# Kernel optimization log

Measured on AMD Instinct MI355X. Metric: run time of the kernel, lower is better.

The kernel has to match this reference:

```python
import jax, jax.numpy as jnp
import numpy as np

WINDOW_SIZE = 11
SIGMA = 1.5
C1 = 0.01 ** 2
C2 = 0.03 ** 2


def _create_window(window_size, channel, dtype):
    coords = jnp.arange(window_size, dtype=jnp.float32) - window_size // 2
    g = jnp.exp(-coords ** 2 / (2.0 * SIGMA ** 2))
    g = g / g.sum()
    win2d = jnp.outer(g, g)  # [k, k]
    # depthwise kernel: [C, 1, k, k] in OIHW with feature_group_count=C
    return jnp.broadcast_to(win2d[None, None], (channel, 1, window_size, window_size)).astype(dtype)


def _dw_conv(x, w, channel):
    pad = WINDOW_SIZE // 2
    return jax.lax.conv_general_dilated(
        x, w,
        window_strides=(1, 1),
        padding=[(pad, pad), (pad, pad)],
        dimension_numbers=('NCHW', 'OIHW', 'NCHW'),
        feature_group_count=channel,
    )


def setup_inputs() -> dict:
    key = jax.random.key(0)
    k1, k2 = jax.random.split(key)
    shape = (16, 3, 512, 512)
    img1 = jax.random.uniform(k1, shape, dtype=jnp.float32)
    img2 = jax.random.uniform(k2, shape, dtype=jnp.float32)
    return {"img1": img1, "img2": img2}


def reference(img1, img2):
    channel = img1.shape[1]
    window = _create_window(WINDOW_SIZE, channel, img1.dtype)

    mu1 = _dw_conv(img1, window, channel)
    mu2 = _dw_conv(img2, window, channel)
    mu1_sq = mu1 * mu1
    mu2_sq = mu2 * mu2
    mu1_mu2 = mu1 * mu2

    sigma1_sq = _dw_conv(img1 * img1, window, channel) - mu1_sq
    sigma2_sq = _dw_conv(img2 * img2, window, channel) - mu2_sq
    sigma12 = _dw_conv(img1 * img2, window, channel) - mu1_mu2

    ssim_map = ((2.0 * mu1_mu2 + C1) * (2.0 * sigma12 + C2)) / (
        (mu1_sq + mu2_sq + C1) * (sigma1_sq + sigma2_sq + C2))
    # forward() returns only the mean SSIM (mcs mean is computed but discarded)
    return ssim_map.mean()
```

## Files before the change

kernel.cpp:

```cpp
#include <hip/hip_runtime.h>
#include <math.h>


#define KW 11
#define RAD 5
#define IMG_W 512
#define IMG_H 512
#define TY 34
#define NJB 4
#define LROW 74
#define C1F 0.0001f
#define C2F 0.0009f

typedef float v2f __attribute__((ext_vector_type(2)));

__global__ __launch_bounds__(256) void ssim_fused_kernel(
    const float* __restrict__ img1,
    const float* __restrict__ img2,
    float* __restrict__ out,
    float inv_n)
{
    __shared__ v2f rows[4][2][LROW];
    __shared__ float red[4];

    const int tid  = threadIdx.x;
    const int lane = tid & 63;
    const int wvi  = tid >> 6;

    const int x0 = (blockIdx.x * 4 + wvi) * 64;
    const int y0 = blockIdx.y * TY;

    const size_t pbase = (size_t)blockIdx.z * (size_t)(IMG_W * IMG_H);
    const float* __restrict__ p1 = img1 + pbase;
    const float* __restrict__ p2 = img2 + pbase;

    float g[KW];
    {
        double t[KW];
        double s = 0.0;
        #pragma unroll
        for (int i = 0; i < KW; ++i) {
            const double c = (double)(i - RAD);
            t[i] = exp(-(c * c) / 4.5);
            s += t[i];
        }
        #pragma unroll
        for (int i = 0; i < KW; ++i) {
            const float gi = (float)(t[i] / s);
            g[i] = __int_as_float(__builtin_amdgcn_readfirstlane(__float_as_int(gi)));
        }
    }

    const int c0   = x0 - RAD + lane;
    const int c0c  = min(max(c0, 0), IMG_W - 1);
    const float m0 = (c0 == c0c) ? 1.f : 0.f;
    const int c1   = c0 + 64;
    const int c1c  = min(max(c1, 0), IMG_W - 1);
    const float m1 = (c1 == c1c) ? 1.f : 0.f;

    auto load_row = [&](int j, v2f& v0, v2f& v1) {
        const int ir = y0 - RAD + j;
        v0 = (v2f){0.f, 0.f};
        v1 = (v2f){0.f, 0.f};
        if ((unsigned)ir < (unsigned)IMG_H) {
            const float* r1 = p1 + ir * IMG_W;
            const float* r2 = p2 + ir * IMG_W;
            v0.x = r1[c0c] * m0;
            v0.y = r2[c0c] * m0;
            if (lane < 2 * RAD) {
                v1.x = r1[c1c] * m1;
                v1.y = r2[c1c] * m1;
            }
        }
    };

    v2f  accMu[KW], accSq[KW];
    float accXy[KW];
    #pragma unroll
    for (int s = 0; s < KW; ++s) {
        accMu[s] = (v2f){0.f, 0.f};
        accSq[s] = (v2f){0.f, 0.f};
        accXy[s] = 0.f;
    }

    v2f cur0, cur1;
    load_row(0, cur0, cur1);

    float acc = 0.f;

    #pragma clang loop unroll(disable)
    for (int jb = 0; jb < NJB; ++jb) {
        #pragma unroll
        for (int P = 0; P < KW; ++P) {
            const int j   = jb * KW + P;
            const int buf = j & 1;
            v2f* __restrict__ wrow = rows[wvi][buf];

            wrow[lane] = cur0;
            if (lane < 2 * RAD) wrow[64 + lane] = cur1;
            __threadfence_block();

            load_row(j + 1, cur0, cur1);

            v2f hmu = (v2f){0.f, 0.f};
            v2f hsq = (v2f){0.f, 0.f};
            float hxy = 0.f;
            #pragma unroll
            for (int k = 0; k < KW; ++k) {
                const v2f ab = wrow[lane + k];
                const v2f w  = g[k] * ab;
                hmu += w;
                hsq = __builtin_elementwise_fma(w, ab, hsq);
                hxy = fmaf(w.x, ab.y, hxy);
            }

            #pragma unroll
            for (int s = 0; s < KW; ++s) {
                const float wt = g[(P - s + KW) % KW];
                const v2f wv2 = (v2f){wt, wt};
                if (s == P) {
                    accMu[s] = wv2 * hmu;
                    accSq[s] = wv2 * hsq;
                    accXy[s] = wt * hxy;
                } else {
                    accMu[s] = __builtin_elementwise_fma(wv2, hmu, accMu[s]);
                    accSq[s] = __builtin_elementwise_fma(wv2, hsq, accSq[s]);
                    accXy[s] = fmaf(wt, hxy, accXy[s]);
                }
            }

            const int oy = y0 + j - 2 * RAD;
            if (j >= 2 * RAD && oy < IMG_H) {
                const int e = (P + 1) % KW;
                const v2f mu    = accMu[e];
                const v2f musq  = mu * mu;
                const float mu12 = mu.x * mu.y;
                const v2f sig   = accSq[e] - musq;
                const float s12 = accXy[e] - mu12;
                const float num = fmaf(2.f, mu12, C1F) * fmaf(2.f, s12, C2F);
                const float den = (musq.x + musq.y + C1F) * (sig.x + sig.y + C2F);
                acc = fmaf(num, __builtin_amdgcn_rcpf(den), acc);
            }
        }
    }

    #pragma unroll
    for (int off = 32; off > 0; off >>= 1)
        acc += __shfl_xor(acc, off, 64);
    if (lane == 0) red[wvi] = acc;
    __syncthreads();
    if (tid == 0) {
        const float s = red[0] + red[1] + red[2] + red[3];
        atomicAdd(out, s * inv_n);
    }
}

extern "C" void kernel_launch(void* const* d_in, const int* in_sizes, int n_in,
                              void* d_out, int out_size, void* d_ws, size_t ws_size,
                              hipStream_t stream) {
    (void)in_sizes; (void)n_in; (void)d_ws; (void)ws_size;
    const float* img1 = (const float*)d_in[0];
    const float* img2 = (const float*)d_in[1];
    float* out = (float*)d_out;

    hipMemsetAsync(out, 0, (size_t)out_size * sizeof(float), stream);

    const float inv_n = 1.0f / (16.0f * 3.0f * 512.0f * 512.0f);
    dim3 grid(2, 16, 16 * 3);
    ssim_fused_kernel<<<grid, dim3(256, 1, 1), 0, stream>>>(img1, img2, out, inv_n);
}
```

Before: 175.2 us.

## Compute two output columns per thread with vectorized loads and summed squares

Each lane now handles two adjacent output columns, so a wave covers 128 columns and a block spans the full image width. Rows are loaded as float2 pairs and staged in LDS as float4, which halves the number of LDS reads per output. Only x²+y² and x·y are accumulated, since SSIM needs only the sum of the two variances, so the separate xx and yy sums are merged. The grid shrinks to 16x48 blocks, which halves the block count. It adds register pressure from four accumulator sets of eleven slots each, which may lower occupancy.

```diff
diff --git a/kernel.cpp b/kernel.cpp
--- a/kernel.cpp
+++ b/kernel.cpp
@@ -8,11 +8,12 @@
 #define IMG_H 512
 #define TY 34
 #define NJB 4
-#define LROW 74
+#define NV4 70
 #define C1F 0.0001f
 #define C2F 0.0009f
 
 typedef float v2f __attribute__((ext_vector_type(2)));
+typedef float v4f __attribute__((ext_vector_type(4)));
 
 __global__ __launch_bounds__(256) void ssim_fused_kernel(
     const float* __restrict__ img1,
@@ -20,17 +21,17 @@
     float* __restrict__ out,
     float inv_n)
 {
-    __shared__ v2f rows[4][2][LROW];
+    __shared__ v4f rows[4][2][NV4];
     __shared__ float red[4];
 
     const int tid  = threadIdx.x;
     const int lane = tid & 63;
     const int wvi  = tid >> 6;
 
-    const int x0 = (blockIdx.x * 4 + wvi) * 64;
-    const int y0 = blockIdx.y * TY;
+    const int x0 = wvi * 128;
+    const int y0 = blockIdx.x * TY;
 
-    const size_t pbase = (size_t)blockIdx.z * (size_t)(IMG_W * IMG_H);
+    const size_t pbase = (size_t)blockIdx.y * (size_t)(IMG_W * IMG_H);
     const float* __restrict__ p1 = img1 + pbase;
     const float* __restrict__ p2 = img2 + pbase;
 
@@ -51,40 +52,42 @@
         }
     }
 
-    const int c0   = x0 - RAD + lane;
-    const int c0c  = min(max(c0, 0), IMG_W - 1);
-    const float m0 = (c0 == c0c) ? 1.f : 0.f;
-    const int c1   = c0 + 64;
-    const int c1c  = min(max(c1, 0), IMG_W - 1);
-    const float m1 = (c1 == c1c) ? 1.f : 0.f;
+    const int cm  = x0 - 6 + 2 * lane;
+    const int cmc = min(max(cm, 0), IMG_W - 2);
+    const float mm0 = (cm     >= 0 && cm     < IMG_W) ? 1.f : 0.f;
+    const float mm1 = (cm + 1 >= 0 && cm + 1 < IMG_W) ? 1.f : 0.f;
+    const int ch  = x0 + 122 + 2 * lane;
+    const int chc = min(max(ch, 0), IMG_W - 2);
+    const float mh0 = (ch     < IMG_W) ? 1.f : 0.f;
+    const float mh1 = (ch + 1 < IMG_W) ? 1.f : 0.f;
 
-    auto load_row = [&](int j, v2f& v0, v2f& v1) {
+    auto load_row = [&](int j, v4f& vm, v4f& vh) {
         const int ir = y0 - RAD + j;
-        v0 = (v2f){0.f, 0.f};
-        v1 = (v2f){0.f, 0.f};
+        vm = (v4f){0.f, 0.f, 0.f, 0.f};
+        vh = (v4f){0.f, 0.f, 0.f, 0.f};
         if ((unsigned)ir < (unsigned)IMG_H) {
             const float* r1 = p1 + ir * IMG_W;
             const float* r2 = p2 + ir * IMG_W;
-            v0.x = r1[c0c] * m0;
-            v0.y = r2[c0c] * m0;
-            if (lane < 2 * RAD) {
-                v1.x = r1[c1c] * m1;
-                v1.y = r2[c1c] * m1;
+            const v2f a = *reinterpret_cast<const v2f*>(r1 + cmc);
+            const v2f b = *reinterpret_cast<const v2f*>(r2 + cmc);
+            vm = (v4f){a.x * mm0, b.x * mm0, a.y * mm1, b.y * mm1};
+            if (lane < 6) {
+                const v2f ah = *reinterpret_cast<const v2f*>(r1 + chc);
+                const v2f bh = *reinterpret_cast<const v2f*>(r2 + chc);
+                vh = (v4f){ah.x * mh0, bh.x * mh0, ah.y * mh1, bh.y * mh1};
             }
         }
     };
 
-    v2f  accMu[KW], accSq[KW];
-    float accXy[KW];
+    v2f aMuA[KW], aSPA[KW], aMuB[KW], aSPB[KW];
     #pragma unroll
     for (int s = 0; s < KW; ++s) {
-        accMu[s] = (v2f){0.f, 0.f};
-        accSq[s] = (v2f){0.f, 0.f};
-        accXy[s] = 0.f;
+        aMuA[s] = (v2f){0.f, 0.f}; aSPA[s] = (v2f){0.f, 0.f};
+        aMuB[s] = (v2f){0.f, 0.f}; aSPB[s] = (v2f){0.f, 0.f};
     }
 
-    v2f cur0, cur1;
-    load_row(0, cur0, cur1);
+    v4f curm, curh;
+    load_row(0, curm, curh);
 
     float acc = 0.f;
 
@@ -94,24 +97,40 @@
         for (int P = 0; P < KW; ++P) {
             const int j   = jb * KW + P;
             const int buf = j & 1;
-            v2f* __restrict__ wrow = rows[wvi][buf];
+            v4f* __restrict__ wrow = rows[wvi][buf];
 
-            wrow[lane] = cur0;
-            if (lane < 2 * RAD) wrow[64 + lane] = cur1;
+            wrow[lane] = curm;
+            if (lane < 6) wrow[64 + lane] = curh;
             __threadfence_block();
 
-            load_row(j + 1, cur0, cur1);
+            load_row(j + 1, curm, curh);
 
-            v2f hmu = (v2f){0.f, 0.f};
-            v2f hsq = (v2f){0.f, 0.f};
-            float hxy = 0.f;
+            v4f e[7];
+            #pragma unroll
+            for (int r = 0; r < 7; ++r) e[r] = wrow[lane + r];
+
+            v2f ab[14], sp[14];
+            #pragma unroll
+            for (int i = 0; i < 14; ++i) {
+                const v4f q = e[i >> 1];
+                const v2f t = (i & 1) ? (v2f){q.z, q.w} : (v2f){q.x, q.y};
+                ab[i] = t;
+            }
+            #pragma unroll
+            for (int i = 1; i <= 12; ++i) {
+                const v2f t = ab[i];
+                sp[i] = (v2f){fmaf(t.x, t.x, t.y * t.y), t.x * t.y};
+            }
+
+            v2f hMuA = (v2f){0.f, 0.f}, hSPA = (v2f){0.f, 0.f};
+            v2f hMuB = (v2f){0.f, 0.f}, hSPB = (v2f){0.f, 0.f};
             #pragma unroll
             for (int k = 0; k < KW; ++k) {
-                const v2f ab = wrow[lane + k];
-                const v2f w  = g[k] * ab;
-                hmu += w;
-                hsq = __builtin_elementwise_fma(w, ab, hsq);
-                hxy = fmaf(w.x, ab.y, hxy);
+                const v2f gk = (v2f){g[k], g[k]};
+                hMuA = __builtin_elementwise_fma(gk, ab[1 + k], hMuA);
+                hSPA = __builtin_elementwise_fma(gk, sp[1 + k], hSPA);
+                hMuB = __builtin_elementwise_fma(gk, ab[2 + k], hMuB);
+                hSPB = __builtin_elementwise_fma(gk, sp[2 + k], hSPB);
             }
 
             #pragma unroll
@@ -119,27 +138,32 @@
                 const float wt = g[(P - s + KW) % KW];
                 const v2f wv2 = (v2f){wt, wt};
                 if (s == P) {
-                    accMu[s] = wv2 * hmu;
-                    accSq[s] = wv2 * hsq;
-                    accXy[s] = wt * hxy;
+                    aMuA[s] = wv2 * hMuA;  aSPA[s] = wv2 * hSPA;
+                    aMuB[s] = wv2 * hMuB;  aSPB[s] = wv2 * hSPB;
                 } else {
-                    accMu[s] = __builtin_elementwise_fma(wv2, hmu, accMu[s]);
-                    accSq[s] = __builtin_elementwise_fma(wv2, hsq, accSq[s]);
-                    accXy[s] = fmaf(wt, hxy, accXy[s]);
+                    aMuA[s] = __builtin_elementwise_fma(wv2, hMuA, aMuA[s]);
+                    aSPA[s] = __builtin_elementwise_fma(wv2, hSPA, aSPA[s]);
+                    aMuB[s] = __builtin_elementwise_fma(wv2, hMuB, aMuB[s]);
+                    aSPB[s] = __builtin_elementwise_fma(wv2, hSPB, aSPB[s]);
                 }
             }
 
             const int oy = y0 + j - 2 * RAD;
             if (j >= 2 * RAD && oy < IMG_H) {
-                const int e = (P + 1) % KW;
-                const v2f mu    = accMu[e];
-                const v2f musq  = mu * mu;
-                const float mu12 = mu.x * mu.y;
-                const v2f sig   = accSq[e] - musq;
-                const float s12 = accXy[e] - mu12;
-                const float num = fmaf(2.f, mu12, C1F) * fmaf(2.f, s12, C2F);
-                const float den = (musq.x + musq.y + C1F) * (sig.x + sig.y + C2F);
-                acc = fmaf(num, __builtin_amdgcn_rcpf(den), acc);
+                const int e2 = (P + 1) % KW;
+                #pragma unroll
+                for (int px = 0; px < 2; ++px) {
+                    const v2f mu = px ? aMuB[e2] : aMuA[e2];
+                    const v2f SP = px ? aSPB[e2] : aSPA[e2];
+                    const v2f musq = mu * mu;
+                    const float mu12  = mu.x * mu.y;
+                    const float musum = musq.x + musq.y;
+                    const float ssum  = SP.x - musum;
+                    const float s12   = SP.y - mu12;
+                    const float num = fmaf(2.f, mu12, C1F) * fmaf(2.f, s12, C2F);
+                    const float den = (musum + C1F) * (ssum + C2F);
+                    acc = fmaf(num, __builtin_amdgcn_rcpf(den), acc);
+                }
             }
         }
     }
@@ -166,6 +190,6 @@
     hipMemsetAsync(out, 0, (size_t)out_size * sizeof(float), stream);
 
     const float inv_n = 1.0f / (16.0f * 3.0f * 512.0f * 512.0f);
-    dim3 grid(2, 16, 16 * 3);
+    dim3 grid(16, 48, 1);
     ssim_fused_kernel<<<grid, dim3(256, 1, 1), 0, stream>>>(img1, img2, out, inv_n);
 }
```

Measured after the change: 152.9 us. -12.7%, faster.

## Merge sigma1+sigma2 into one sum channel and use explicit LDS waitcnt

Applied to the files above, without the earlier changes.

Because SSIM only needs sigma1_sq + sigma2_sq, the two squared-image convolutions are merged into a single channel (x^2+y^2) and paired with x*y in one v2f. This cuts the vertical accumulators from five to four floats per slot and lowers register pressure and FMA count. It also replaces the block threadfence with an explicit lgkmcnt wait and adds a min-waves launch bound of 4. The merge changes summation order slightly, and the register-limiting launch bound could cause spills.

```diff
diff --git a/kernel.cpp b/kernel.cpp
--- a/kernel.cpp
+++ b/kernel.cpp
@@ -14,7 +14,7 @@
 
 typedef float v2f __attribute__((ext_vector_type(2)));
 
-__global__ __launch_bounds__(256) void ssim_fused_kernel(
+__global__ __launch_bounds__(256, 4) void ssim_fused_kernel(
     const float* __restrict__ img1,
     const float* __restrict__ img2,
     float* __restrict__ out,
@@ -57,34 +57,29 @@
     const int c1   = c0 + 64;
     const int c1c  = min(max(c1, 0), IMG_W - 1);
     const float m1 = (c1 == c1c) ? 1.f : 0.f;
+    const bool halo = (lane < 2 * RAD);
 
-    auto load_row = [&](int j, v2f& v0, v2f& v1) {
+    auto load_row = [&](int j, v2f& vm, v2f& vh) {
         const int ir = y0 - RAD + j;
-        v0 = (v2f){0.f, 0.f};
-        v1 = (v2f){0.f, 0.f};
+        vm = (v2f){0.f, 0.f};
+        vh = (v2f){0.f, 0.f};
         if ((unsigned)ir < (unsigned)IMG_H) {
             const float* r1 = p1 + ir * IMG_W;
             const float* r2 = p2 + ir * IMG_W;
-            v0.x = r1[c0c] * m0;
-            v0.y = r2[c0c] * m0;
-            if (lane < 2 * RAD) {
-                v1.x = r1[c1c] * m1;
-                v1.y = r2[c1c] * m1;
-            }
+            vm = (v2f){r1[c0c] * m0, r2[c0c] * m0};
+            if (halo) vh = (v2f){r1[c1c] * m1, r2[c1c] * m1};
         }
     };
 
-    v2f  accMu[KW], accSq[KW];
-    float accXy[KW];
+    v2f aMu[KW], aSP[KW];
     #pragma unroll
     for (int s = 0; s < KW; ++s) {
-        accMu[s] = (v2f){0.f, 0.f};
-        accSq[s] = (v2f){0.f, 0.f};
-        accXy[s] = 0.f;
+        aMu[s] = (v2f){0.f, 0.f};
+        aSP[s] = (v2f){0.f, 0.f};
     }
 
-    v2f cur0, cur1;
-    load_row(0, cur0, cur1);
+    v2f curm, curh;
+    load_row(0, curm, curh);
 
     float acc = 0.f;
 
@@ -96,22 +91,21 @@
             const int buf = j & 1;
             v2f* __restrict__ wrow = rows[wvi][buf];
 
-            wrow[lane] = cur0;
-            if (lane < 2 * RAD) wrow[64 + lane] = cur1;
-            __threadfence_block();
+            wrow[lane] = curm;
+            if (halo) wrow[64 + lane] = curh;
+            asm volatile("s_waitcnt lgkmcnt(0)" ::: "memory");
 
-            load_row(j + 1, cur0, cur1);
+            load_row(j + 1, curm, curh);
 
-            v2f hmu = (v2f){0.f, 0.f};
-            v2f hsq = (v2f){0.f, 0.f};
-            float hxy = 0.f;
+            v2f hMu = (v2f){0.f, 0.f};
+            v2f hSP = (v2f){0.f, 0.f};
             #pragma unroll
             for (int k = 0; k < KW; ++k) {
-                const v2f ab = wrow[lane + k];
-                const v2f w  = g[k] * ab;
-                hmu += w;
-                hsq = __builtin_elementwise_fma(w, ab, hsq);
-                hxy = fmaf(w.x, ab.y, hxy);
+                const v2f t = wrow[lane + k];
+                const v2f gk = (v2f){g[k], g[k]};
+                const v2f spv = (v2f){fmaf(t.x, t.x, t.y * t.y), t.x * t.y};
+                hMu = __builtin_elementwise_fma(gk, t,   hMu);
+                hSP = __builtin_elementwise_fma(gk, spv, hSP);
             }
 
             #pragma unroll
@@ -119,26 +113,26 @@
                 const float wt = g[(P - s + KW) % KW];
                 const v2f wv2 = (v2f){wt, wt};
                 if (s == P) {
-                    accMu[s] = wv2 * hmu;
-                    accSq[s] = wv2 * hsq;
-                    accXy[s] = wt * hxy;
+                    aMu[s] = wv2 * hMu;
+                    aSP[s] = wv2 * hSP;
                 } else {
-                    accMu[s] = __builtin_elementwise_fma(wv2, hmu, accMu[s]);
-                    accSq[s] = __builtin_elementwise_fma(wv2, hsq, accSq[s]);
-                    accXy[s] = fmaf(wt, hxy, accXy[s]);
+                    aMu[s] = __builtin_elementwise_fma(wv2, hMu, aMu[s]);
+                    aSP[s] = __builtin_elementwise_fma(wv2, hSP, aSP[s]);
                 }
             }
 
             const int oy = y0 + j - 2 * RAD;
             if (j >= 2 * RAD && oy < IMG_H) {
-                const int e = (P + 1) % KW;
-                const v2f mu    = accMu[e];
-                const v2f musq  = mu * mu;
-                const float mu12 = mu.x * mu.y;
-                const v2f sig   = accSq[e] - musq;
-                const float s12 = accXy[e] - mu12;
+                const int e2 = (P + 1) % KW;
+                const v2f mu = aMu[e2];
+                const v2f SP = aSP[e2];
+                const v2f musq = mu * mu;
+                const float mu12  = mu.x * mu.y;
+                const float musum = musq.x + musq.y;
+                const float ssum  = SP.x - musum;
+                const float s12   = SP.y - mu12;
                 const float num = fmaf(2.f, mu12, C1F) * fmaf(2.f, s12, C2F);
-                const float den = (musq.x + musq.y + C1F) * (sig.x + sig.y + C2F);
+                const float den = (musum + C1F) * (ssum + C2F);
                 acc = fmaf(num, __builtin_amdgcn_rcpf(den), acc);
             }
         }
@@ -166,6 +160,6 @@
     hipMemsetAsync(out, 0, (size_t)out_size * sizeof(float), stream);
 
     const float inv_n = 1.0f / (16.0f * 3.0f * 512.0f * 512.0f);
-    dim3 grid(2, 16, 16 * 3);
+    dim3 grid(2, 16, 48);
     ssim_fused_kernel<<<grid, dim3(256, 1, 1), 0, stream>>>(img1, img2, out, inv_n);
 }
```

Result: slower. 185.5 us (+5.9%).
